# Performance work log

Measured on AMD Instinct MI355X. Metric: run time of the kernel, lower is better.

## Reference

```python
import jax, jax.numpy as jnp
import numpy as np

B, S, D, H = 2, 4096, 128, 128
EPS = 1e-6
NEG_INF = -1e30


def _complex_linear(xr, xi, Wr, Wi, br, bi):
    # x: (B,S,D); W: (H,D); complex linear (Wr + i Wi)(xr + i xi) + (br + i bi) per layer math:
    # real_out = (xr Wr + br) - (xi Wi + bi); imag_out = (xi Wr + br) + (xr Wi + bi)
    out_r = xr @ Wr.T + br - (xi @ Wi.T + bi)
    out_i = xi @ Wr.T + br + (xr @ Wi.T + bi)
    return out_r, out_i


def setup_inputs() -> dict:
    key = jax.random.key(0)
    ks = jax.random.split(key, 24)
    scale = 1.0 / np.sqrt(D)
    def W(k):
        return jax.random.normal(k, (H, D), jnp.float32) * scale
    def b(k):
        return jax.random.normal(k, (H,), jnp.float32) * 0.01
    inp = {
        "Z_q": jax.random.normal(ks[0], (B, 2, S, D, 1), jnp.float32),
        "Z_k": jax.random.normal(ks[1], (B, 2, S, D, 1), jnp.float32),
        "Z_v": jax.random.normal(ks[2], (B, 2, S, D, 1), jnp.float32),
        "Wq_r": W(ks[3]), "Wq_i": W(ks[4]), "bq_r": b(ks[5]), "bq_i": b(ks[6]),
        "Wk_r": W(ks[7]), "Wk_i": W(ks[8]), "bk_r": b(ks[9]), "bk_i": b(ks[10]),
        "Wv_r": W(ks[11]), "Wv_i": W(ks[12]), "bv_r": b(ks[13]), "bv_i": b(ks[14]),
        "Wp_r": W(ks[15]), "Wp_i": W(ks[16]), "bp_r": b(ks[17]), "bp_i": b(ks[18]),
        "noise_floor": jnp.asarray(1.0, jnp.float32),
        "tau": jnp.asarray(0.0, jnp.float32),
    }
    return inp


def reference(Z_q, Z_k, Z_v,
              Wq_r, Wq_i, bq_r, bq_i,
              Wk_r, Wk_i, bk_r, bk_i,
              Wv_r, Wv_i, bv_r, bv_i,
              Wp_r, Wp_i, bp_r, bp_i,
              noise_floor, tau):
    # squeeze trailing singleton; split real/imag -> (B,S,D)
    zqr, zqi = Z_q[:, 0, :, :, 0], Z_q[:, 1, :, :, 0]
    zkr, zki = Z_k[:, 0, :, :, 0], Z_k[:, 1, :, :, 0]
    zvr, zvi = Z_v[:, 0, :, :, 0], Z_v[:, 1, :, :, 0]

    Qr, Qi = _complex_linear(zqr, zqi, Wq_r, Wq_i, bq_r, bq_i)
    Kr, Ki = _complex_linear(zkr, zki, Wk_r, Wk_i, bk_r, bk_i)
    Vr, Vi = _complex_linear(zvr, zvi, Wv_r, Wv_i, bv_r, bv_i)

    # InverseMahalanobis: R2[b,i,j] = sum_h |Q[b,i]-K[b,j]|^2
    q2 = jnp.sum(Qr * Qr + Qi * Qi, axis=-1)          # (B,S)
    k2 = jnp.sum(Kr * Kr + Ki * Ki, axis=-1)          # (B,S)
    re_qk = (jnp.einsum('bsh,bth->bst', Qr, Kr)
             + jnp.einsum('bsh,bth->bst', Qi, Ki))    # (B,S,S)
    R2 = q2[:, :, None] + k2[:, None, :] - 2.0 * re_qk

    attn_scores = -jax.nn.softplus(tau) * jnp.log(noise_floor ** 2 + R2 + EPS)
    mask = jnp.tril(jnp.ones((S, S), dtype=bool))[None]
    attn_scores = jnp.where(mask, attn_scores, NEG_INF)
    attn_weights = jax.nn.softmax(attn_scores / jnp.sqrt(jnp.float32(H)), axis=-1)

    # attn (real) times complex V
    est_r = jnp.einsum('bst,bth->bsh', attn_weights, Vr)
    est_i = jnp.einsum('bst,bth->bsh', attn_weights, Vi)

    out_r, out_i = _complex_linear(est_r, est_i, Wp_r, Wp_i, bp_r, bp_i)
    out = jnp.stack((out_r, out_i), axis=1)[..., None]  # (B,2,S,H,1)
    return out, attn_weights
```

## Files before the change

kernel.cpp:

```cpp
#include <hip/hip_runtime.h>

#define S_LEN 4096
#define NBATCH 2
#define ROWS (NBATCH*S_LEN)
#define OUT_ELEMS 2097152

typedef _Float16 f16;
typedef _Float16 f16x8 __attribute__((ext_vector_type(8)));
typedef _Float16 f16x4 __attribute__((ext_vector_type(4)));
typedef float f32x4 __attribute__((ext_vector_type(4)));

#define MT_OFF    0x000000
#define BIAS_OFF  0x080000
#define SC_OFF    0x081000
#define QH_OFF    0x100000
#define KH_OFF    0x500000
#define VT_OFF    0x900000
#define Q2_OFF    0xD00000
#define K2_OFF    0xD10000
#define L_OFF     0xD20000
#define EST_OFF   0xE00000
#define PW_OFF    0x1600000
#define WS_NEED   0x5600000

#define MFMA16(A,B,C) __builtin_amdgcn_mfma_f32_16x16x32_f16(A,B,C,0,0,0)

__device__ __forceinline__ void async_cp16(f16* lds, const f16* g) {
  __builtin_amdgcn_global_load_lds(
      (const __attribute__((address_space(1))) void*)g,
      (__attribute__((address_space(3))) void*)lds, 16, 0, 0);
}

__device__ __forceinline__ void stage16(f16* lds, const f16* g, int stride, int tid) {
#pragma unroll
  for (int i = 0; i < 2; ++i) {
    int idx = i*256 + tid;
    int row = idx >> 2, c = idx & 3;
    async_cp16(lds + idx*8, g + (size_t)row*stride + c*8);
  }
}

__device__ __forceinline__ void stage32(f16* lds, const float* g, int stride, int tid,
                                        const float* rowscale) {
#pragma unroll
  for (int i = 0; i < 4; ++i) {
    int idx = i*256 + tid;
    int row = idx >> 3, c = idx & 7;
    const float4* gp = (const float4*)(g + (size_t)row*stride + c*4);
    float4 v = *gp;
    float sc = rowscale ? rowscale[row] : 1.0f;
    f16x4 h; h[0]=(f16)(v.x*sc); h[1]=(f16)(v.y*sc); h[2]=(f16)(v.z*sc); h[3]=(f16)(v.w*sc);
    *(f16x4*)(lds + row*32 + c*4) = h;
  }
}

__device__ __forceinline__ void mfma_step(const f16* Asm, const f16* Bsm, int lane,
                                          int wm, int wn, f32x4 acc[4][4]) {
  f16x8 a[4], b[4];
  int rr = lane & 15, kk = (lane >> 4) << 3;
#pragma unroll
  for (int i=0;i<4;i++) a[i] = *(const f16x8*)(Asm + (wm + i*16 + rr)*32 + kk);
#pragma unroll
  for (int j=0;j<4;j++) b[j] = *(const f16x8*)(Bsm + (wn + j*16 + rr)*32 + kk);
#pragma unroll
  for (int i=0;i<4;i++)
#pragma unroll
    for (int j=0;j<4;j++) acc[i][j] = MFMA16(a[i], b[j], acc[i][j]);
}

__global__ __launch_bounds__(256)
void k_build(const float* Wqr, const float* Wqi, const float* bqr, const float* bqi,
             const float* Wkr, const float* Wki, const float* bkr, const float* bki,
             const float* Wvr, const float* Wvi, const float* bvr, const float* bvi,
             const float* Wpr, const float* Wpi, const float* bpr, const float* bpi,
             f16* Mt, float* bias) {
  int mat = blockIdx.x;
  const float *Wr, *Wi, *br, *bi;
  if (mat == 0)      { Wr=Wqr; Wi=Wqi; br=bqr; bi=bqi; }
  else if (mat == 1) { Wr=Wkr; Wi=Wki; br=bkr; bi=bki; }
  else if (mat == 2) { Wr=Wvr; Wi=Wvi; br=bvr; bi=bvi; }
  else               { Wr=Wpr; Wi=Wpi; br=bpr; bi=bpi; }
  int idx = blockIdx.y*256 + threadIdx.x;
  int n = idx >> 8, k = idx & 255;
  int d = k & 127, h = n & 127;
  float w = (k < 128) ? ((n < 128) ? Wr[h*128+d] : Wi[h*128+d])
                      : ((n < 128) ? -Wi[h*128+d] : Wr[h*128+d]);
  Mt[mat*65536 + n*256 + k] = (f16)w;
  if (k == 0)
    bias[mat*256 + n] = (n < 128) ? (br[n] - bi[n]) : (br[n-128] + bi[n-128]);
}

__global__ __launch_bounds__(256)
void k_init(float* est, float* zreg, float* sc, const float* nf, const float* tau) {
  int idx = blockIdx.x*256 + threadIdx.x;
  if (idx < 524288) ((float4*)est)[idx] = make_float4(0.f,0.f,0.f,0.f);
  else { int j = idx - 524288; if (j < 12288) ((float4*)zreg)[j] = make_float4(0.f,0.f,0.f,0.f); }
  if (idx == 0) {
    float t = tau[0];
    float c = __builtin_log2f(1.0f + __builtin_exp2f(t * 1.4426950408889634f))
              * 0.6931471805599453f;
    sc[0] = -c * 0.08838834764831845f;
    sc[1] = nf[0]*nf[0] + 1e-6f;
  }
}

__global__ __launch_bounds__(256)
void k_proj(const float* Zq, const float* Zk, const float* Zv,
            const f16* Mt, const float* bias,
            f16* Qh, f16* Kh, f16* Vt, float* q2, float* k2) {
  __shared__ f16 Asm[128*32];
  __shared__ f16 Bsm[128*32];
  __shared__ float bias_s[128];
  int tid = threadIdx.x;
  int mode = blockIdx.z;
  int m0 = blockIdx.x * 128, n0 = blockIdx.y * 128;
  const float* Z = (mode==0) ? Zq : (mode==1 ? Zk : Zv);
  const f16* Bt = Mt + mode*65536;
  if (tid < 128) bias_s[tid] = bias[mode*256 + n0 + tid];
  int b = m0 >> 12, s0 = m0 & 4095;
  int lane = tid & 63, w = tid >> 6;
  int wm = (w >> 1)*64, wn = (w & 1)*64;
  f32x4 acc[4][4] = {};
  for (int kb = 0; kb < 8; ++kb) {
    int k0 = kb*32;
    int part = k0 >> 7, d0 = k0 & 127;
    const float* Ag = Z + (((size_t)(b*2 + part))*S_LEN + s0)*128 + d0;
    stage32(Asm, Ag, 128, tid, nullptr);
    stage16(Bsm, Bt + n0*256 + k0, 256, tid);
    __syncthreads();
    mfma_step(Asm, Bsm, lane, wm, wn, acc);
    __syncthreads();
  }
  int rr = (lane>>4)*4, cc = lane & 15;
  if (mode < 2) {
    f16* O = (mode==0) ? Qh : Kh;
    float rs[4][4];
#pragma unroll
    for (int i=0;i<4;i++)
#pragma unroll
      for (int r=0;r<4;r++) rs[i][r]=0.f;
#pragma unroll
    for (int i=0;i<4;i++)
#pragma unroll
      for (int j=0;j<4;j++) {
        int cl = wn + j*16 + cc;
        int cg = n0 + cl;
        float bv = bias_s[cl];
#pragma unroll
        for (int r=0;r<4;r++) {
          int rg = m0 + wm + i*16 + rr + r;
          f16 hv = (f16)(acc[i][j][r] + bv);
          O[(size_t)rg*256 + cg] = hv;
          float fv = (float)hv;
          rs[i][r] += fv*fv;
        }
      }
#pragma unroll
    for (int m=8;m>=1;m>>=1)
#pragma unroll
      for (int i=0;i<4;i++)
#pragma unroll
        for (int r=0;r<4;r++) rs[i][r] += __shfl_xor(rs[i][r], m, 64);
    if (cc == 0) {
      float* T = (mode==0) ? q2 : k2;
#pragma unroll
      for (int i=0;i<4;i++)
#pragma unroll
        for (int r=0;r<4;r++) {
          int rg = m0 + wm + i*16 + rr + r;
          atomicAdd(&T[rg], rs[i][r]);
        }
    }
  } else {
#pragma unroll
    for (int i=0;i<4;i++) {
      int t0 = s0 + wm + i*16 + rr;
#pragma unroll
      for (int j=0;j<4;j++) {
        int cl = wn + j*16 + cc;
        int cg = n0 + cl;
        float bv = bias_s[cl];
        f16x4 h4;
#pragma unroll
        for (int r=0;r<4;r++) h4[r] = (f16)(acc[i][j][r] + bv);
        *(f16x4*)(Vt + (size_t)b*1048576 + (size_t)cg*4096 + t0) = h4;
      }
    }
  }
}

__global__ __launch_bounds__(256)
void k_attn(const f16* Qh, const f16* Kh, const float* q2, const float* k2,
            const float* sc, float* lsum, f16* Pws, float* attn) {
  int x = blockIdx.x;
  int b = x >> 10, r = x & 1023;
  int sb = r >> 5, tb = r & 31;
  int s0 = sb*128, t0 = tb*128;
  int tid = threadIdx.x;
  if (tb > sb) {
    float4 z = make_float4(0.f,0.f,0.f,0.f);
    int row = tid >> 1, h = tid & 1;
    float4* p = (float4*)(attn + ((size_t)(b*S_LEN) + s0 + row)*S_LEN + t0 + h*64);
#pragma unroll
    for (int i=0;i<16;i++) p[i] = z;
    return;
  }
  __shared__ f16 Asm[128*32];
  __shared__ f16 Bsm[128*32];
  __shared__ float q2s[128], k2s[128];
  if (tid < 128) {
    q2s[tid] = q2[b*S_LEN + s0 + tid];
    k2s[tid] = k2[b*S_LEN + t0 + tid];
  }
  float kc = sc[0], nf2 = sc[1];
  int lane = tid & 63, w = tid >> 6;
  int wm = (w >> 1)*64, wn = (w & 1)*64;
  const f16* Ag = Qh + ((size_t)(b*S_LEN) + s0)*256;
  const f16* Bg = Kh + ((size_t)(b*S_LEN) + t0)*256;
  f32x4 acc[4][4] = {};
  for (int kb=0;kb<8;kb++) {
    stage16(Asm, Ag + kb*32, 256, tid);
    stage16(Bsm, Bg + kb*32, 256, tid);
    __syncthreads();
    mfma_step(Asm, Bsm, lane, wm, wn, acc);
    __syncthreads();
  }
  int rr = (lane>>4)*4, cc = lane & 15;
  bool diag = (tb == sb);
  float rs[4][4];
#pragma unroll
  for (int i=0;i<4;i++)
#pragma unroll
    for (int rg=0;rg<4;rg++) rs[i][rg]=0.f;
#pragma unroll
  for (int i=0;i<4;i++)
#pragma unroll
    for (int j=0;j<4;j++) {
      int cl = wn + j*16 + cc;
      float kv = k2s[cl];
#pragma unroll
      for (int rg=0;rg<4;rg++) {
        int rl = wm + i*16 + rr + rg;
        float xx = nf2 + q2s[rl] + kv - 2.0f*acc[i][j][rg];
        float P = __builtin_exp2f(kc * __builtin_log2f(__builtin_fmaxf(xx, 1e-6f)));
        if (diag && (t0+cl) > (s0+rl)) P = 0.f;
        Pws[((size_t)(b*S_LEN) + s0 + rl)*S_LEN + t0 + cl] = (f16)P;
        rs[i][rg] += P;
      }
    }
#pragma unroll
  for (int m=8;m>=1;m>>=1)
#pragma unroll
    for (int i=0;i<4;i++)
#pragma unroll
      for (int rg=0;rg<4;rg++) rs[i][rg] += __shfl_xor(rs[i][rg], m, 64);
  if (cc == 0)
#pragma unroll
    for (int i=0;i<4;i++)
#pragma unroll
      for (int rg=0;rg<4;rg++) {
        int rl = wm + i*16 + rr + rg;
        atomicAdd(&lsum[b*S_LEN + s0 + rl], rs[i][rg]);
      }
}

__global__ __launch_bounds__(256)
void k_pv(const f16* Pws, const f16* Vt, const float* lsum, float* est, float* attn) {
  __shared__ f16 Asm[128*32];
  __shared__ f16 Bsm[128*32];
  __shared__ float ls[128];
  int r = blockIdx.x;
  int nb = blockIdx.y, b = blockIdx.z;
  int sb = 0;
  while (r >= ((sb+4)>>2)) { r -= (sb+4)>>2; sb++; }
  int c = r;
  int s0 = sb*128, h0 = nb*128;
  int tid = threadIdx.x;
  bool wrb = (nb == 0);
  if (wrb && tid < 128) ls[tid] = 1.0f / lsum[b*S_LEN + s0 + tid];
  int lane = tid & 63, w = tid >> 6;
  int wm = (w>>1)*64, wn = (w&1)*64;
  int tb0 = c*4, tb1 = tb0 + 4; if (tb1 > sb+1) tb1 = sb+1;
  const f16* Abase = Pws + ((size_t)(b*S_LEN) + s0)*S_LEN;
  const f16* Bbase = Vt + (size_t)b*1048576 + (size_t)h0*4096;
  f32x4 acc[4][4] = {};
  int row2 = tid >> 1, half2 = tid & 1;
  for (int tb = tb0; tb < tb1; ++tb)
    for (int kk = 0; kk < 4; ++kk) {
      int t0 = tb*128 + kk*32;
      stage16(Asm, Abase + t0, S_LEN, tid);
      stage16(Bsm, Bbase + t0, 4096, tid);
      __syncthreads();
      if (wrb) {
        float invl = ls[row2];
        const f16x8* src = (const f16x8*)(Asm + row2*32 + half2*16);
        f16x8 v0 = src[0], v1 = src[1];
        float4* dst = (float4*)(attn + ((size_t)(b*S_LEN) + s0 + row2)*S_LEN + t0 + half2*16);
        float4 o;
        o.x=(float)v0[0]*invl; o.y=(float)v0[1]*invl; o.z=(float)v0[2]*invl; o.w=(float)v0[3]*invl; dst[0]=o;
        o.x=(float)v0[4]*invl; o.y=(float)v0[5]*invl; o.z=(float)v0[6]*invl; o.w=(float)v0[7]*invl; dst[1]=o;
        o.x=(float)v1[0]*invl; o.y=(float)v1[1]*invl; o.z=(float)v1[2]*invl; o.w=(float)v1[3]*invl; dst[2]=o;
        o.x=(float)v1[4]*invl; o.y=(float)v1[5]*invl; o.z=(float)v1[6]*invl; o.w=(float)v1[7]*invl; dst[3]=o;
      }
      mfma_step(Asm, Bsm, lane, wm, wn, acc);
      __syncthreads();
    }
  int rr = (lane>>4)*4, cc = lane & 15;
#pragma unroll
  for (int i=0;i<4;i++)
#pragma unroll
    for (int j=0;j<4;j++) {
      int cg = h0 + wn + j*16 + cc;
#pragma unroll
      for (int rg=0;rg<4;rg++) {
        int rgl = s0 + wm + i*16 + rr + rg;
        atomicAdd(&est[((size_t)(b*S_LEN) + rgl)*256 + cg], acc[i][j][rg]);
      }
    }
}

__global__ __launch_bounds__(256)
void k_out(const float* est, const f16* Mt, const float* bias, const float* lsum,
           float* outp) {
  __shared__ f16 Asm[128*32];
  __shared__ f16 Bsm[128*32];
  __shared__ float bias_s[128];
  __shared__ float ls[128];
  int m0 = blockIdx.x*128, n0 = blockIdx.y*128;
  int tid = threadIdx.x;
  int b = m0 >> 12, s0 = m0 & 4095;
  if (tid < 128) {
    bias_s[tid] = bias[3*256 + n0 + tid];
    ls[tid] = 1.0f / lsum[b*S_LEN + s0 + tid];
  }
  __syncthreads();
  int lane = tid & 63, w = tid >> 6;
  int wm = (w>>1)*64, wn = (w&1)*64;
  const f16* Bt = Mt + 3*65536;
  f32x4 acc[4][4] = {};
  for (int kb=0;kb<8;kb++) {
    stage32(Asm, est + (size_t)m0*256 + kb*32, 256, tid, ls);
    stage16(Bsm, Bt + n0*256 + kb*32, 256, tid);
    __syncthreads();
    mfma_step(Asm, Bsm, lane, wm, wn, acc);
    __syncthreads();
  }
  int rr = (lane>>4)*4, cc = lane & 15;
#pragma unroll
  for (int i=0;i<4;i++)
#pragma unroll
    for (int j=0;j<4;j++) {
      int cl = wn + j*16 + cc;
      int cg = n0 + cl;
      int comp = cg >> 7, h = cg & 127;
      float bv = bias_s[cl];
#pragma unroll
      for (int rg=0;rg<4;rg++) {
        int s = s0 + wm + i*16 + rr + rg;
        outp[(((size_t)(b*2 + comp))*S_LEN + s)*128 + h] = acc[i][j][rg] + bv;
      }
    }
}

extern "C" void kernel_launch(void* const* d_in, const int* in_sizes, int n_in,
                              void* d_out, int out_size, void* d_ws, size_t ws_size,
                              hipStream_t stream) {
  (void)in_sizes; (void)n_in; (void)out_size;
  if (ws_size < (size_t)WS_NEED) return;
  const float* Zq = (const float*)d_in[0];
  const float* Zk = (const float*)d_in[1];
  const float* Zv = (const float*)d_in[2];
  char* ws = (char*)d_ws;
  f16*   Mt   = (f16*)(ws + MT_OFF);
  float* bias = (float*)(ws + BIAS_OFF);
  float* sc   = (float*)(ws + SC_OFF);
  f16*   Qh   = (f16*)(ws + QH_OFF);
  f16*   Kh   = (f16*)(ws + KH_OFF);
  f16*   Vt   = (f16*)(ws + VT_OFF);
  float* q2   = (float*)(ws + Q2_OFF);
  float* k2   = (float*)(ws + K2_OFF);
  float* lsum = (float*)(ws + L_OFF);
  float* est  = (float*)(ws + EST_OFF);
  f16*   Pws  = (f16*)(ws + PW_OFF);
  float* outp = (float*)d_out;
  float* attn = outp + OUT_ELEMS;

  k_build<<<dim3(4,256), 256, 0, stream>>>(
      (const float*)d_in[3],  (const float*)d_in[4],  (const float*)d_in[5],  (const float*)d_in[6],
      (const float*)d_in[7],  (const float*)d_in[8],  (const float*)d_in[9],  (const float*)d_in[10],
      (const float*)d_in[11], (const float*)d_in[12], (const float*)d_in[13], (const float*)d_in[14],
      (const float*)d_in[15], (const float*)d_in[16], (const float*)d_in[17], (const float*)d_in[18],
      Mt, bias);
  k_init<<<2096, 256, 0, stream>>>(est, q2, sc, (const float*)d_in[19], (const float*)d_in[20]);
  k_proj<<<dim3(64,2,3), 256, 0, stream>>>(Zq, Zk, Zv, Mt, bias, Qh, Kh, Vt, q2, k2);
  k_attn<<<2048, 256, 0, stream>>>(Qh, Kh, q2, k2, sc, lsum, Pws, attn);
  k_pv<<<dim3(144,2,2), 256, 0, stream>>>(Pws, Vt, lsum, est, attn);
  k_out<<<dim3(64,2), 256, 0, stream>>>(est, Mt, bias, lsum, outp);
}
```

Measured before the change: 302.1 us.

## Split attn normalization into its own kernel, launch only causal tiles, halve proj tiles

```diff
diff --git a/kernel.cpp b/kernel.cpp
--- a/kernel.cpp
+++ b/kernel.cpp
@@ -31,19 +31,21 @@
       (__attribute__((address_space(3))) void*)lds, 16, 0, 0);
 }
 
+template<int TR>
 __device__ __forceinline__ void stage16(f16* lds, const f16* g, int stride, int tid) {
 #pragma unroll
-  for (int i = 0; i < 2; ++i) {
+  for (int i = 0; i < TR/64; ++i) {
     int idx = i*256 + tid;
     int row = idx >> 2, c = idx & 3;
     async_cp16(lds + idx*8, g + (size_t)row*stride + c*8);
   }
 }
 
+template<int TR>
 __device__ __forceinline__ void stage32(f16* lds, const float* g, int stride, int tid,
                                         const float* rowscale) {
 #pragma unroll
-  for (int i = 0; i < 4; ++i) {
+  for (int i = 0; i < TR/32; ++i) {
     int idx = i*256 + tid;
     int row = idx >> 3, c = idx & 7;
     const float4* gp = (const float4*)(g + (size_t)row*stride + c*4);
@@ -54,18 +56,19 @@
   }
 }
 
+template<int MI, int NJ>
 __device__ __forceinline__ void mfma_step(const f16* Asm, const f16* Bsm, int lane,
-                                          int wm, int wn, f32x4 acc[4][4]) {
-  f16x8 a[4], b[4];
+                                          int wm, int wn, f32x4 (&acc)[MI][NJ]) {
+  f16x8 a[MI], b[NJ];
   int rr = lane & 15, kk = (lane >> 4) << 3;
 #pragma unroll
-  for (int i=0;i<4;i++) a[i] = *(const f16x8*)(Asm + (wm + i*16 + rr)*32 + kk);
-#pragma unroll
-  for (int j=0;j<4;j++) b[j] = *(const f16x8*)(Bsm + (wn + j*16 + rr)*32 + kk);
-#pragma unroll
-  for (int i=0;i<4;i++)
-#pragma unroll
-    for (int j=0;j<4;j++) acc[i][j] = MFMA16(a[i], b[j], acc[i][j]);
+  for (int i=0;i<MI;i++) a[i] = *(const f16x8*)(Asm + (wm + i*16 + rr)*32 + kk);
+#pragma unroll
+  for (int j=0;j<NJ;j++) b[j] = *(const f16x8*)(Bsm + (wn + j*16 + rr)*32 + kk);
+#pragma unroll
+  for (int i=0;i<MI;i++)
+#pragma unroll
+    for (int j=0;j<NJ;j++) acc[i][j] = MFMA16(a[i], b[j], acc[i][j]);
 }
 
 __global__ __launch_bounds__(256)
@@ -108,39 +111,39 @@
 void k_proj(const float* Zq, const float* Zk, const float* Zv,
             const f16* Mt, const float* bias,
             f16* Qh, f16* Kh, f16* Vt, float* q2, float* k2) {
-  __shared__ f16 Asm[128*32];
+  __shared__ f16 Asm[64*32];
   __shared__ f16 Bsm[128*32];
   __shared__ float bias_s[128];
   int tid = threadIdx.x;
   int mode = blockIdx.z;
-  int m0 = blockIdx.x * 128, n0 = blockIdx.y * 128;
+  int m0 = blockIdx.x * 64, n0 = blockIdx.y * 128;
   const float* Z = (mode==0) ? Zq : (mode==1 ? Zk : Zv);
   const f16* Bt = Mt + mode*65536;
   if (tid < 128) bias_s[tid] = bias[mode*256 + n0 + tid];
   int b = m0 >> 12, s0 = m0 & 4095;
   int lane = tid & 63, w = tid >> 6;
-  int wm = (w >> 1)*64, wn = (w & 1)*64;
-  f32x4 acc[4][4] = {};
+  int wm = (w >> 1)*32, wn = (w & 1)*64;
+  f32x4 acc[2][4] = {};
   for (int kb = 0; kb < 8; ++kb) {
     int k0 = kb*32;
     int part = k0 >> 7, d0 = k0 & 127;
     const float* Ag = Z + (((size_t)(b*2 + part))*S_LEN + s0)*128 + d0;
-    stage32(Asm, Ag, 128, tid, nullptr);
-    stage16(Bsm, Bt + n0*256 + k0, 256, tid);
-    __syncthreads();
-    mfma_step(Asm, Bsm, lane, wm, wn, acc);
+    stage32<64>(Asm, Ag, 128, tid, nullptr);
+    stage16<128>(Bsm, Bt + n0*256 + k0, 256, tid);
+    __syncthreads();
+    mfma_step<2,4>(Asm, Bsm, lane, wm, wn, acc);
     __syncthreads();
   }
   int rr = (lane>>4)*4, cc = lane & 15;
   if (mode < 2) {
     f16* O = (mode==0) ? Qh : Kh;
-    float rs[4][4];
-#pragma unroll
-    for (int i=0;i<4;i++)
+    float rs[2][4];
+#pragma unroll
+    for (int i=0;i<2;i++)
 #pragma unroll
       for (int r=0;r<4;r++) rs[i][r]=0.f;
 #pragma unroll
-    for (int i=0;i<4;i++)
+    for (int i=0;i<2;i++)
 #pragma unroll
       for (int j=0;j<4;j++) {
         int cl = wn + j*16 + cc;
@@ -158,13 +161,13 @@
 #pragma unroll
     for (int m=8;m>=1;m>>=1)
 #pragma unroll
-      for (int i=0;i<4;i++)
+      for (int i=0;i<2;i++)
 #pragma unroll
         for (int r=0;r<4;r++) rs[i][r] += __shfl_xor(rs[i][r], m, 64);
     if (cc == 0) {
       float* T = (mode==0) ? q2 : k2;
 #pragma unroll
-      for (int i=0;i<4;i++)
+      for (int i=0;i<2;i++)
 #pragma unroll
         for (int r=0;r<4;r++) {
           int rg = m0 + wm + i*16 + rr + r;
@@ -173,7 +176,7 @@
     }
   } else {
 #pragma unroll
-    for (int i=0;i<4;i++) {
+    for (int i=0;i<2;i++) {
       int t0 = s0 + wm + i*16 + rr;
 #pragma unroll
       for (int j=0;j<4;j++) {
@@ -191,23 +194,18 @@
 
 __global__ __launch_bounds__(256)
 void k_attn(const f16* Qh, const f16* Kh, const float* q2, const float* k2,
-            const float* sc, float* lsum, f16* Pws, float* attn) {
-  int x = blockIdx.x;
-  int b = x >> 10, r = x & 1023;
-  int sb = r >> 5, tb = r & 31;
-  int s0 = sb*128, t0 = tb*128;
-  int tid = threadIdx.x;
-  if (tb > sb) {
-    float4 z = make_float4(0.f,0.f,0.f,0.f);
-    int row = tid >> 1, h = tid & 1;
-    float4* p = (float4*)(attn + ((size_t)(b*S_LEN) + s0 + row)*S_LEN + t0 + h*64);
-#pragma unroll
-    for (int i=0;i<16;i++) p[i] = z;
-    return;
-  }
+            const float* sc, float* lsum, f16* Pws) {
   __shared__ f16 Asm[128*32];
   __shared__ f16 Bsm[128*32];
   __shared__ float q2s[128], k2s[128];
+  int x = blockIdx.x;
+  int b = x / 528, r = x % 528;
+  int sb = (int)((__builtin_sqrtf(8.f*(float)r + 1.f) - 1.f)*0.5f);
+  while ((sb+1)*(sb+2)/2 <= r) sb++;
+  while (sb*(sb+1)/2 > r) sb--;
+  int tb = r - sb*(sb+1)/2;
+  int s0 = sb*128, t0 = tb*128;
+  int tid = threadIdx.x;
   if (tid < 128) {
     q2s[tid] = q2[b*S_LEN + s0 + tid];
     k2s[tid] = k2[b*S_LEN + t0 + tid];
@@ -219,10 +217,10 @@
   const f16* Bg = Kh + ((size_t)(b*S_LEN) + t0)*256;
   f32x4 acc[4][4] = {};
   for (int kb=0;kb<8;kb++) {
-    stage16(Asm, Ag + kb*32, 256, tid);
-    stage16(Bsm, Bg + kb*32, 256, tid);
-    __syncthreads();
-    mfma_step(Asm, Bsm, lane, wm, wn, acc);
+    stage16<128>(Asm, Ag + kb*32, 256, tid);
+    stage16<128>(Bsm, Bg + kb*32, 256, tid);
+    __syncthreads();
+    mfma_step<4,4>(Asm, Bsm, lane, wm, wn, acc);
     __syncthreads();
   }
   int rr = (lane>>4)*4, cc = lane & 15;
@@ -265,10 +263,9 @@
 }
 
 __global__ __launch_bounds__(256)
-void k_pv(const f16* Pws, const f16* Vt, const float* lsum, float* est, float* attn) {
+void k_pv(const f16* Pws, const f16* Vt, float* est) {
   __shared__ f16 Asm[128*32];
   __shared__ f16 Bsm[128*32];
-  __shared__ float ls[128];
   int r = blockIdx.x;
   int nb = blockIdx.y, b = blockIdx.z;
   int sb = 0;
@@ -276,33 +273,19 @@
   int c = r;
   int s0 = sb*128, h0 = nb*128;
   int tid = threadIdx.x;
-  bool wrb = (nb == 0);
-  if (wrb && tid < 128) ls[tid] = 1.0f / lsum[b*S_LEN + s0 + tid];
   int lane = tid & 63, w = tid >> 6;
   int wm = (w>>1)*64, wn = (w&1)*64;
   int tb0 = c*4, tb1 = tb0 + 4; if (tb1 > sb+1) tb1 = sb+1;
   const f16* Abase = Pws + ((size_t)(b*S_LEN) + s0)*S_LEN;
   const f16* Bbase = Vt + (size_t)b*1048576 + (size_t)h0*4096;
   f32x4 acc[4][4] = {};
-  int row2 = tid >> 1, half2 = tid & 1;
   for (int tb = tb0; tb < tb1; ++tb)
     for (int kk = 0; kk < 4; ++kk) {
       int t0 = tb*128 + kk*32;
-      stage16(Asm, Abase + t0, S_LEN, tid);
-      stage16(Bsm, Bbase + t0, 4096, tid);
+      stage16<128>(Asm, Abase + t0, S_LEN, tid);
+      stage16<128>(Bsm, Bbase + t0, 4096, tid);
       __syncthreads();
-      if (wrb) {
-        float invl = ls[row2];
-        const f16x8* src = (const f16x8*)(Asm + row2*32 + half2*16);
-        f16x8 v0 = src[0], v1 = src[1];
-        float4* dst = (float4*)(attn + ((size_t)(b*S_LEN) + s0 + row2)*S_LEN + t0 + half2*16);
-        float4 o;
-        o.x=(float)v0[0]*invl; o.y=(float)v0[1]*invl; o.z=(float)v0[2]*invl; o.w=(float)v0[3]*invl; dst[0]=o;
-        o.x=(float)v0[4]*invl; o.y=(float)v0[5]*invl; o.z=(float)v0[6]*invl; o.w=(float)v0[7]*invl; dst[1]=o;
-        o.x=(float)v1[0]*invl; o.y=(float)v1[1]*invl; o.z=(float)v1[2]*invl; o.w=(float)v1[3]*invl; dst[2]=o;
-        o.x=(float)v1[4]*invl; o.y=(float)v1[5]*invl; o.z=(float)v1[6]*invl; o.w=(float)v1[7]*invl; dst[3]=o;
-      }
-      mfma_step(Asm, Bsm, lane, wm, wn, acc);
+      mfma_step<4,4>(Asm, Bsm, lane, wm, wn, acc);
       __syncthreads();
     }
   int rr = (lane>>4)*4, cc = lane & 15;
@@ -320,34 +303,51 @@
 }
 
 __global__ __launch_bounds__(256)
+void k_norm(const f16* __restrict__ Pws, const float* __restrict__ lsum,
+            float* __restrict__ attn) {
+  int lin = blockIdx.x*256 + threadIdx.x;
+  int row = lin >> 10, t4 = lin & 1023;
+  int srow = row & 4095;
+  int t0 = t4 << 2;
+  float4 o = make_float4(0.f,0.f,0.f,0.f);
+  if (t0 <= srow) {
+    float invl = 1.0f / lsum[row];
+    f16x4 p = *(const f16x4*)(Pws + ((size_t)row<<12) + t0);
+    o.x = (float)p[0]*invl;
+    o.y = (t0+1 <= srow) ? (float)p[1]*invl : 0.f;
+    o.z = (t0+2 <= srow) ? (float)p[2]*invl : 0.f;
+    o.w = (t0+3 <= srow) ? (float)p[3]*invl : 0.f;
+  }
+  ((float4*)attn)[lin] = o;
+}
+
+__global__ __launch_bounds__(256)
 void k_out(const float* est, const f16* Mt, const float* bias, const float* lsum,
            float* outp) {
-  __shared__ f16 Asm[128*32];
+  __shared__ f16 Asm[64*32];
   __shared__ f16 Bsm[128*32];
   __shared__ float bias_s[128];
-  __shared__ float ls[128];
-  int m0 = blockIdx.x*128, n0 = blockIdx.y*128;
+  __shared__ float ls[64];
+  int m0 = blockIdx.x*64, n0 = blockIdx.y*128;
   int tid = threadIdx.x;
   int b = m0 >> 12, s0 = m0 & 4095;
-  if (tid < 128) {
-    bias_s[tid] = bias[3*256 + n0 + tid];
-    ls[tid] = 1.0f / lsum[b*S_LEN + s0 + tid];
-  }
+  if (tid < 128) bias_s[tid] = bias[3*256 + n0 + tid];
+  if (tid < 64)  ls[tid] = 1.0f / lsum[b*S_LEN + s0 + tid];
   __syncthreads();
   int lane = tid & 63, w = tid >> 6;
-  int wm = (w>>1)*64, wn = (w&1)*64;
+  int wm = (w>>1)*32, wn = (w&1)*64;
   const f16* Bt = Mt + 3*65536;
-  f32x4 acc[4][4] = {};
+  f32x4 acc[2][4] = {};
   for (int kb=0;kb<8;kb++) {
-    stage32(Asm, est + (size_t)m0*256 + kb*32, 256, tid, ls);
-    stage16(Bsm, Bt + n0*256 + kb*32, 256, tid);
-    __syncthreads();
-    mfma_step(Asm, Bsm, lane, wm, wn, acc);
+    stage32<64>(Asm, est + (size_t)m0*256 + kb*32, 256, tid, ls);
+    stage16<128>(Bsm, Bt + n0*256 + kb*32, 256, tid);
+    __syncthreads();
+    mfma_step<2,4>(Asm, Bsm, lane, wm, wn, acc);
     __syncthreads();
   }
   int rr = (lane>>4)*4, cc = lane & 15;
 #pragma unroll
-  for (int i=0;i<4;i++)
+  for (int i=0;i<2;i++)
 #pragma unroll
     for (int j=0;j<4;j++) {
       int cl = wn + j*16 + cc;
@@ -392,8 +392,9 @@
       (const float*)d_in[15], (const float*)d_in[16], (const float*)d_in[17], (const float*)d_in[18],
       Mt, bias);
   k_init<<<2096, 256, 0, stream>>>(est, q2, sc, (const float*)d_in[19], (const float*)d_in[20]);
-  k_proj<<<dim3(64,2,3), 256, 0, stream>>>(Zq, Zk, Zv, Mt, bias, Qh, Kh, Vt, q2, k2);
-  k_attn<<<2048, 256, 0, stream>>>(Qh, Kh, q2, k2, sc, lsum, Pws, attn);
-  k_pv<<<dim3(144,2,2), 256, 0, stream>>>(Pws, Vt, lsum, est, attn);
-  k_out<<<dim3(64,2), 256, 0, stream>>>(est, Mt, bias, lsum, outp);
-}
+  k_proj<<<dim3(128,2,3), 256, 0, stream>>>(Zq, Zk, Zv, Mt, bias, Qh, Kh, Vt, q2, k2);
+  k_attn<<<1056, 256, 0, stream>>>(Qh, Kh, q2, k2, sc, lsum, Pws);
+  k_pv<<<dim3(144,2,2), 256, 0, stream>>>(Pws, Vt, est);
+  k_norm<<<32768, 256, 0, stream>>>(Pws, lsum, attn);
+  k_out<<<dim3(128,2), 256, 0, stream>>>(est, Mt, bias, lsum, outp);
+}
```

Measured after the change: 310.3 us. +2.7%, slower.
